# Performance work log

Hardware: AMD Instinct MI355X
Metric: run time of the kernel (lower is better)

The kernel has to match this reference:

```python
import jax, jax.numpy as jnp
import numpy as np

B, S, D, E = 16, 2048, 1024, 524288

def setup_inputs() -> dict:
    key = jax.random.key(0)
    k0, k1, k2, k3 = jax.random.split(key, 4)
    x = jax.random.normal(k0, (B, S, D), dtype=jnp.float32)
    mask = jnp.ones((B, S), dtype=bool)
    edges = jax.random.randint(k1, (2, E), 0, B * S, dtype=jnp.int32)
    scale = 1.0 / np.sqrt(D).astype(np.float32)
    W1 = jax.random.normal(k2, (D, D), dtype=jnp.float32) * scale  # GCNConv lin weight
    b1 = jnp.zeros((D,), dtype=jnp.float32)                        # GCNConv bias
    W2 = jax.random.normal(k3, (D, D), dtype=jnp.float32) * scale  # output Linear
    b2 = jnp.zeros((D,), dtype=jnp.float32)
    return {"x": x, "mask": mask, "edges": edges, "W1": W1, "b1": b1, "W2": W2, "b2": b2}

def reference(x, mask, edges, W1, b1, W2, b2):
    # x: [B,S,D]; mask all-True -> gather == reshape to [N,D]
    N = B * S
    nodes = x.reshape(N, D)
    src, dst = edges[0], edges[1]
    # GCN normalization (gcn_norm, add_self_loops=False): deg over dst, norm = d^-1/2[src]*d^-1/2[dst]
    deg = jax.ops.segment_sum(jnp.ones((E,), dtype=nodes.dtype), dst, num_segments=N)
    dinv = jnp.where(deg > 0, jax.lax.rsqrt(jnp.maximum(deg, 1e-12)), 0.0)
    norm = dinv[src] * dinv[dst]  # [E]
    h = nodes @ W1.T                                   # [N,D] transform
    msg = h[src] * norm[:, None]                       # [E,D] gather + scale
    agg = jax.ops.segment_sum(msg, dst, num_segments=N) + b1  # scatter-aggregate + bias
    g = jax.nn.gelu(agg, approximate=False)            # nn.GELU (exact erf)
    out = g @ W2.T + b2                                # Linear(graph_hid_dim -> input_dim)
    # residual scatter-add back into x (mask all True)
    return x + (out.reshape(B, S, D) * mask[:, :, None].astype(x.dtype))
```

## Files before the change

### kernel.cpp

```cpp
#include <hip/hip_runtime.h>
#include <hip/hip_fp8.h>
#include <stdint.h>

typedef unsigned short u16;
typedef __attribute__((ext_vector_type(8))) short s16x8;
typedef __attribute__((ext_vector_type(4))) float f32x4;
typedef __attribute__((ext_vector_type(2))) float f32x2;

#define D_DIM 1024
#define GK 1024
#define NT 16

__device__ __forceinline__ u16 f2bf(float f) {
  union { float f; uint32_t u; } v; v.f = f;
  uint32_t u = v.u;
  return (u16)((u + 0x7FFFu + ((u >> 16) & 1u)) >> 16);
}

__device__ __forceinline__ uint8_t f2fp8(float f) {
#if __has_builtin(__builtin_amdgcn_cvt_pk_fp8_f32)
  int p = __builtin_amdgcn_cvt_pk_fp8_f32(f, f, 0, false);
  return (uint8_t)(p & 0xff);
#else
  return __hip_fp8_e4m3(f).__x;
#endif
}


__device__ __forceinline__ int lds_half_off(int arr, int buf, int half) {
  return ((((arr << 1) | buf) << 1) | half) << 14;
}

__device__ __forceinline__ void stage_half(const u16* __restrict__ g, int rowBase, int kt,
                                           u16* lds, int arr, int buf, int half, int t) {
  const int hoff = lds_half_off(arr, buf, half);
#pragma unroll
  for (int j = 0; j < 2; ++j) {
    const int c = j * 512 + t;
    const int row = c >> 3;
    const int cb = (((c & 7) ^ (row & 7)) << 4);
    const u16* src = g + (size_t)(rowBase + half * 128 + row) * GK + kt * 64 + (cb >> 1);
    __builtin_amdgcn_global_load_lds((const __attribute__((address_space(1))) void*)src,
        (__attribute__((address_space(3))) void*)((char*)lds + hoff + c * 16), 16, 0, 0);
  }
}

template<int QM>
__device__ __forceinline__ void read_sub_a(const u16* lds, int buf, int half, int lane, s16x8* a) {
  const int base = lds_half_off(0, buf, half);
  const int rsel = lane & 15, cb0 = (lane >> 4) << 4;
#pragma unroll
  for (int im = 0; im < 4; ++im) {
    const int row = QM * 64 + im * 16 + rsel;
    const int swz = (row & 7) << 4;
#pragma unroll
    for (int ks = 0; ks < 2; ++ks)
      a[im * 2 + ks] = *(const s16x8*)((const char*)lds + base + row * 128 + ((ks * 64 + cb0) ^ swz));
  }
}

template<int QN>
__device__ __forceinline__ void read_sub_b(const u16* lds, int buf, int half, int rowBase, int lane, s16x8* b) {
  const int base = lds_half_off(1, buf, half);
  const int rsel = lane & 15, cb0 = (lane >> 4) << 4;
#pragma unroll
  for (int in_ = 0; in_ < 2; ++in_) {
    const int row = rowBase + (QN * 2 + in_) * 16 + rsel;
    const int swz = (row & 7) << 4;
#pragma unroll
    for (int ks = 0; ks < 2; ++ks)
      b[in_ * 2 + ks] = *(const s16x8*)((const char*)lds + base + row * 128 + ((ks * 64 + cb0) ^ swz));
  }
}

template<int QM, int QN>
__device__ __forceinline__ void do_quad(f32x4 acc[8][4], const s16x8* aS, const s16x8* bS) {
  __builtin_amdgcn_s_setprio(1);
#pragma unroll
  for (int im = 0; im < 4; ++im)
#pragma unroll
    for (int in_ = 0; in_ < 2; ++in_)
#pragma unroll
      for (int ks = 0; ks < 2; ++ks)
        acc[QM * 4 + im][QN * 2 + in_] = __builtin_amdgcn_mfma_f32_16x16x32_bf16(
            aS[im * 2 + ks], bS[in_ * 2 + ks], acc[QM * 4 + im][QN * 2 + in_], 0, 0, 0);
  __builtin_amdgcn_s_setprio(0);
}

#define BARRIER __builtin_amdgcn_s_barrier()
#define WAIT_LGKM asm volatile("s_waitcnt lgkmcnt(0)" ::: "memory")
#define WAIT_VM(n) asm volatile("s_waitcnt vmcnt(" #n ")" ::: "memory")

template<int EPI>
__global__ __launch_bounds__(512, 2) void gemm256(
    const u16* __restrict__ A, const u16* __restrict__ B, uint8_t* __restrict__ C8,
    const float* __restrict__ bias, const float* __restrict__ xres, float* __restrict__ Cf)
{
  __shared__ u16 lds[65536];
  const int t = threadIdx.x;
  const int lane = t & 63;
  const int w = t >> 6;
  const int wave_m = w >> 2;
  const int wave_n = w & 3;
  const int halfB = wave_n >> 1;
  const int rowBaseB = (wave_n & 1) * 64;

  const int lb = blockIdx.x;
  const int wid = ((lb & 7) << 6) | (lb >> 3);
  const int bm = wid >> 2;
  const int bn = wid & 3;
  const int rowA = bm * 256;
  const int rowB = bn * 256;

  f32x4 acc[8][4] = {};
  s16x8 aS[8], b0S[4], b1S[4];

  stage_half(A, rowA, 0, lds, 0, 0, 0, t);
  stage_half(A, rowA, 0, lds, 0, 0, 1, t);
  stage_half(B, rowB, 0, lds, 1, 0, 0, t);
  stage_half(B, rowB, 0, lds, 1, 0, 1, t);
  stage_half(B, rowB, 1, lds, 1, 1, 0, t);
  stage_half(B, rowB, 1, lds, 1, 1, 1, t);
  WAIT_VM(4);
  BARRIER;

  for (int i = 0; i < NT / 2 - 1; ++i) {
    const int t1 = 2 * i + 1;
    read_sub_a<0>(lds, 0, wave_m, lane, aS);
    read_sub_b<0>(lds, 0, halfB, rowBaseB, lane, b0S);
    stage_half(A, rowA, t1, lds, 0, 1, 0, t);
    BARRIER; WAIT_LGKM;
    do_quad<0, 0>(acc, aS, b0S);
    BARRIER;
    read_sub_b<1>(lds, 0, halfB, rowBaseB, lane, b1S);
    stage_half(A, rowA, t1, lds, 0, 1, 1, t);
    BARRIER; WAIT_LGKM;
    do_quad<0, 1>(acc, aS, b1S);
    BARRIER;
    read_sub_a<1>(lds, 0, wave_m, lane, aS);
    stage_half(B, rowB, 2 * i + 2, lds, 1, 0, 0, t);
    BARRIER; WAIT_LGKM;
    do_quad<1, 1>(acc, aS, b1S);
    BARRIER;
    stage_half(B, rowB, 2 * i + 2, lds, 1, 0, 1, t);
    WAIT_VM(4);
    BARRIER;
    do_quad<1, 0>(acc, aS, b0S);
    BARRIER;
    read_sub_a<0>(lds, 1, wave_m, lane, aS);
    read_sub_b<0>(lds, 1, halfB, rowBaseB, lane, b0S);
    stage_half(A, rowA, 2 * i + 2, lds, 0, 0, 0, t);
    BARRIER; WAIT_LGKM;
    do_quad<0, 0>(acc, aS, b0S);
    BARRIER;
    read_sub_b<1>(lds, 1, halfB, rowBaseB, lane, b1S);
    stage_half(A, rowA, 2 * i + 2, lds, 0, 0, 1, t);
    BARRIER; WAIT_LGKM;
    do_quad<0, 1>(acc, aS, b1S);
    BARRIER;
    read_sub_a<1>(lds, 1, wave_m, lane, aS);
    stage_half(B, rowB, 2 * i + 3, lds, 1, 1, 0, t);
    BARRIER; WAIT_LGKM;
    do_quad<1, 1>(acc, aS, b1S);
    BARRIER;
    stage_half(B, rowB, 2 * i + 3, lds, 1, 1, 1, t);
    WAIT_VM(4);
    BARRIER;
    do_quad<1, 0>(acc, aS, b0S);
    BARRIER;
  }

  {
    read_sub_a<0>(lds, 0, wave_m, lane, aS);
    read_sub_b<0>(lds, 0, halfB, rowBaseB, lane, b0S);
    stage_half(A, rowA, NT - 1, lds, 0, 1, 0, t);
    BARRIER; WAIT_LGKM;
    do_quad<0, 0>(acc, aS, b0S);
    BARRIER;
    read_sub_b<1>(lds, 0, halfB, rowBaseB, lane, b1S);
    stage_half(A, rowA, NT - 1, lds, 0, 1, 1, t);
    BARRIER; WAIT_LGKM;
    do_quad<0, 1>(acc, aS, b1S);
    BARRIER;
    read_sub_a<1>(lds, 0, wave_m, lane, aS);
    BARRIER; WAIT_LGKM;
    do_quad<1, 1>(acc, aS, b1S);
    BARRIER;
    WAIT_VM(0);
    BARRIER;
    do_quad<1, 0>(acc, aS, b0S);
    read_sub_a<0>(lds, 1, wave_m, lane, aS);
    read_sub_b<0>(lds, 1, halfB, rowBaseB, lane, b0S);
    WAIT_LGKM;
    do_quad<0, 0>(acc, aS, b0S);
    read_sub_b<1>(lds, 1, halfB, rowBaseB, lane, b1S);
    WAIT_LGKM;
    do_quad<0, 1>(acc, aS, b1S);
    read_sub_a<1>(lds, 1, wave_m, lane, aS);
    WAIT_LGKM;
    do_quad<1, 1>(acc, aS, b1S);
    do_quad<1, 0>(acc, aS, b0S);
  }

  const int row0 = rowA + wave_m * 128 + ((lane >> 4) << 2);
  const int col0 = rowB + wave_n * 64 + (lane & 15);
  if (EPI == 0) {
#pragma unroll
    for (int mf = 0; mf < 8; ++mf)
#pragma unroll
      for (int nf = 0; nf < 4; ++nf) {
        const int c = col0 + nf * 16;
#pragma unroll
        for (int r = 0; r < 4; ++r)
          C8[(size_t)(row0 + mf * 16 + r) * D_DIM + c] = f2fp8(acc[mf][nf][r]);
      }
  } else {
#pragma unroll
    for (int mf = 0; mf < 8; ++mf)
#pragma unroll
      for (int nf = 0; nf < 4; ++nf) {
        const int c = col0 + nf * 16;
        const float bv = bias[c];
#pragma unroll
        for (int r = 0; r < 4; ++r) {
          const size_t idx = (size_t)(row0 + mf * 16 + r) * D_DIM + c;
          Cf[idx] = acc[mf][nf][r] + bv + xres[idx];
        }
      }
  }
}

__global__ void cast_f32_bf16(const float* __restrict__ in, u16* __restrict__ out, long n) {
  long i = ((long)blockIdx.x * blockDim.x + threadIdx.x) * 4;
  if (i >= n) return;
  const float4 v = *(const float4*)(in + i);
  ushort4 o;
  o.x = f2bf(v.x); o.y = f2bf(v.y); o.z = f2bf(v.z); o.w = f2bf(v.w);
  *(ushort4*)(out + i) = o;
}

__global__ void deg_count_int(const int* __restrict__ dst, int* __restrict__ cnt, int E) {
  int i = blockIdx.x * blockDim.x + threadIdx.x;
  if (i < E) atomicAdd(&cnt[dst[i]], 1);
}

__global__ __launch_bounds__(1024) void scan_offsets(const int* __restrict__ cnt,
                                                     int* __restrict__ off,
                                                     int* __restrict__ cursor,
                                                     float* __restrict__ dinv, int N) {
  __shared__ int part[1024];
  const int t = threadIdx.x;
  const int nper = (N + 1023) / 1024;
  const int base = t * nper;
  int s = 0;
  for (int i = 0; i < nper; ++i) {
    int idx = base + i;
    if (idx < N) s += cnt[idx];
  }
  part[t] = s;
  __syncthreads();
  for (int d = 1; d < 1024; d <<= 1) {
    int v = (t >= d) ? part[t - d] : 0;
    __syncthreads();
    part[t] += v;
    __syncthreads();
  }
  int run = (t > 0) ? part[t - 1] : 0;
  for (int i = 0; i < nper; ++i) {
    int idx = base + i;
    if (idx < N) {
      const int c = cnt[idx];
      off[idx] = run;
      cursor[idx] = run;
      dinv[idx] = c > 0 ? rsqrtf((float)c) : 0.f;
      run += c;
    }
  }
  if (t == 1023) off[N] = run;
}

__global__ void fill_csr(const int* __restrict__ src, const int* __restrict__ dst,
                         const float* __restrict__ dinv, int* __restrict__ cursor,
                         uint2* __restrict__ ebuf, int E) {
  int e = blockIdx.x * blockDim.x + threadIdx.x;
  if (e >= E) return;
  const int d = dst[e], s = src[e];
  const int pos = atomicAdd(&cursor[d], 1);
  const float nrm = dinv[s] * dinv[d];
  uint2 en; en.x = (unsigned)s; en.y = __float_as_uint(nrm);
  ebuf[pos] = en;
}

__device__ __forceinline__ void acc8_fp8(float* a, uint2 hv, float nrm) {
#if __has_builtin(__builtin_amdgcn_cvt_pk_f32_fp8)
  const f32x2 p0 = __builtin_amdgcn_cvt_pk_f32_fp8(hv.x, false);
  const f32x2 p1 = __builtin_amdgcn_cvt_pk_f32_fp8(hv.x, true);
  const f32x2 p2 = __builtin_amdgcn_cvt_pk_f32_fp8(hv.y, false);
  const f32x2 p3 = __builtin_amdgcn_cvt_pk_f32_fp8(hv.y, true);
  a[0] += p0.x * nrm; a[1] += p0.y * nrm;
  a[2] += p1.x * nrm; a[3] += p1.y * nrm;
  a[4] += p2.x * nrm; a[5] += p2.y * nrm;
  a[6] += p3.x * nrm; a[7] += p3.y * nrm;
#else
  const float s = nrm * 0x1p+120f;
#pragma unroll
  for (int k = 0; k < 8; ++k) {
    const uint32_t word = (k < 4) ? hv.x : hv.y;
    const uint32_t b = (word >> ((k & 3) * 8)) & 0xffu;
    a[k] += __uint_as_float(((b & 0x80u) << 24) | ((b & 0x7fu) << 20)) * s;
  }
#endif
}

__device__ __forceinline__ float gelu_exact(float t) {
  return 0.5f * t * (1.0f + erff(t * 0.70710678118f));
}

__global__ __launch_bounds__(256) void aggregate_gelu_fp8(
    const uint8_t* __restrict__ h8, const uint2* __restrict__ ebuf,
    const int* __restrict__ off, const float* __restrict__ b1,
    u16* __restrict__ g)
{
  const int node = __builtin_amdgcn_readfirstlane(blockIdx.x * 2 + (threadIdx.x >> 7));
  const int lt = threadIdx.x & 127;
  const int fb = lt * 8;
  const int beg = off[node], end = off[node + 1];
  float a[8] = {0.f, 0.f, 0.f, 0.f, 0.f, 0.f, 0.f, 0.f};

  int i = beg;
  for (; i + 2 <= end; i += 2) {
    const uint2 ea = ebuf[i];
    const uint2 eb = ebuf[i + 1];
    const uint2 ha = *(const uint2*)(h8 + (size_t)ea.x * D_DIM + fb);
    const uint2 hb = *(const uint2*)(h8 + (size_t)eb.x * D_DIM + fb);
    acc8_fp8(a, ha, __uint_as_float(ea.y));
    acc8_fp8(a, hb, __uint_as_float(eb.y));
  }
  if (i < end) {
    const uint2 ea = ebuf[i];
    const uint2 ha = *(const uint2*)(h8 + (size_t)ea.x * D_DIM + fb);
    acc8_fp8(a, ha, __uint_as_float(ea.y));
  }

  const float4 bA = *(const float4*)(b1 + fb);
  const float4 bB = *(const float4*)(b1 + fb + 4);
  const float v0 = gelu_exact(a[0] + bA.x), v1 = gelu_exact(a[1] + bA.y);
  const float v2 = gelu_exact(a[2] + bA.z), v3 = gelu_exact(a[3] + bA.w);
  const float v4 = gelu_exact(a[4] + bB.x), v5 = gelu_exact(a[5] + bB.y);
  const float v6 = gelu_exact(a[6] + bB.z), v7 = gelu_exact(a[7] + bB.w);
  uint4 o;
  o.x = (uint32_t)f2bf(v0) | ((uint32_t)f2bf(v1) << 16);
  o.y = (uint32_t)f2bf(v2) | ((uint32_t)f2bf(v3) << 16);
  o.z = (uint32_t)f2bf(v4) | ((uint32_t)f2bf(v5) << 16);
  o.w = (uint32_t)f2bf(v6) | ((uint32_t)f2bf(v7) << 16);
  *(uint4*)(g + (size_t)node * D_DIM + fb) = o;
}

extern "C" void kernel_launch(void* const* d_in, const int* in_sizes, int n_in,
                              void* d_out, int out_size, void* d_ws, size_t ws_size,
                              hipStream_t stream) {
  const float* x  = (const float*)d_in[0];
  const int* edges = (const int*)d_in[2];
  const float* W1 = (const float*)d_in[3];
  const float* b1 = (const float*)d_in[4];
  const float* W2 = (const float*)d_in[5];
  const float* b2 = (const float*)d_in[6];
  float* out = (float*)d_out;

  const int D = D_DIM;
  const long ND = (long)in_sizes[0];
  const int N = (int)(ND / D);
  const int E = in_sizes[2] / 2;
  const int* src = edges;
  const int* dst = edges + E;

  u16* xbf    = (u16*)d_ws;
  uint8_t* h8 = (uint8_t*)(xbf + ND);
  u16* w1b    = (u16*)(h8 + ND);
  u16* w2b    = w1b + (size_t)D * D;
  int* cnt    = (int*)(w2b + (size_t)D * D);
  int* off    = cnt + N;
  int* cursor = off + N + 1;
  float* dnv  = (float*)(cursor + N);
  uint2* ebuf = (uint2*)(dnv + N + 1);

  hipMemsetAsync(cnt, 0, (size_t)N * sizeof(int), stream);

  cast_f32_bf16<<<(int)(ND / 4 / 256), 256, 0, stream>>>(x, xbf, ND);
  cast_f32_bf16<<<(int)((long)D * D / 4 / 256), 256, 0, stream>>>(W1, w1b, (long)D * D);
  cast_f32_bf16<<<(int)((long)D * D / 4 / 256), 256, 0, stream>>>(W2, w2b, (long)D * D);

  deg_count_int<<<(E + 255) / 256, 256, 0, stream>>>(dst, cnt, E);
  scan_offsets<<<1, 1024, 0, stream>>>(cnt, off, cursor, dnv, N);
  fill_csr<<<(E + 255) / 256, 256, 0, stream>>>(src, dst, dnv, cursor, ebuf, E);

  gemm256<0><<<(N / 256) * (D / 256), 512, 0, stream>>>(xbf, w1b, h8, nullptr, nullptr, nullptr);

  aggregate_gelu_fp8<<<N / 2, 256, 0, stream>>>(h8, ebuf, off, b1, xbf);

  gemm256<1><<<(N / 256) * (D / 256), 512, 0, stream>>>(xbf, w2b, nullptr, b2, x, out);
}
```

Baseline: 443.5 us.

## Make GEMM blocks persistent over two M-tiles with a continuous K pipeline

```diff
diff --git a/kernel.cpp b/kernel.cpp
--- a/kernel.cpp
+++ b/kernel.cpp
@@ -9,7 +9,7 @@
 
 #define D_DIM 1024
 #define GK 1024
-#define NT 16
+#define NT2 32
 
 __device__ __forceinline__ u16 f2bf(float f) {
   union { float f; uint32_t u; } v; v.f = f;
@@ -31,7 +31,7 @@
   return ((((arr << 1) | buf) << 1) | half) << 14;
 }
 
-__device__ __forceinline__ void stage_half(const u16* __restrict__ g, int rowBase, int kt,
+__device__ __forceinline__ void stage_half(const u16* __restrict__ g, int rowBase, int ktl,
                                            u16* lds, int arr, int buf, int half, int t) {
   const int hoff = lds_half_off(arr, buf, half);
 #pragma unroll
@@ -39,7 +39,7 @@
     const int c = j * 512 + t;
     const int row = c >> 3;
     const int cb = (((c & 7) ^ (row & 7)) << 4);
-    const u16* src = g + (size_t)(rowBase + half * 128 + row) * GK + kt * 64 + (cb >> 1);
+    const u16* src = g + (size_t)(rowBase + half * 128 + row) * GK + ktl * 64 + (cb >> 1);
     __builtin_amdgcn_global_load_lds((const __attribute__((address_space(1))) void*)src,
         (__attribute__((address_space(3))) void*)((char*)lds + hoff + c * 16), 16, 0, 0);
   }
@@ -90,6 +90,39 @@
 #define BARRIER __builtin_amdgcn_s_barrier()
 #define WAIT_LGKM asm volatile("s_waitcnt lgkmcnt(0)" ::: "memory")
 #define WAIT_VM(n) asm volatile("s_waitcnt vmcnt(" #n ")" ::: "memory")
+
+template<int EPI>
+__device__ __forceinline__ void write_tile(const f32x4 (&acc)[8][4], int rowBase, int colBase,
+    uint8_t* __restrict__ C8, const float* __restrict__ bias, const float* __restrict__ xres,
+    float* __restrict__ Cf, int lane, int wave_m, int wave_n)
+{
+  const int row0 = rowBase + wave_m * 128 + ((lane >> 4) << 2);
+  const int col0 = colBase + wave_n * 64 + (lane & 15);
+  if (EPI == 0) {
+#pragma unroll
+    for (int mf = 0; mf < 8; ++mf)
+#pragma unroll
+      for (int nf = 0; nf < 4; ++nf) {
+        const int c = col0 + nf * 16;
+#pragma unroll
+        for (int r = 0; r < 4; ++r)
+          C8[(size_t)(row0 + mf * 16 + r) * D_DIM + c] = f2fp8(acc[mf][nf][r]);
+      }
+  } else {
+#pragma unroll
+    for (int mf = 0; mf < 8; ++mf)
+#pragma unroll
+      for (int nf = 0; nf < 4; ++nf) {
+        const int c = col0 + nf * 16;
+        const float bv = bias[c];
+#pragma unroll
+        for (int r = 0; r < 4; ++r) {
+          const size_t idx = (size_t)(row0 + mf * 16 + r) * D_DIM + c;
+          Cf[idx] = acc[mf][nf][r] + bv + xres[idx];
+        }
+      }
+  }
+}
 
 template<int EPI>
 __global__ __launch_bounds__(512, 2) void gemm256(
@@ -105,80 +138,92 @@
   const int halfB = wave_n >> 1;
   const int rowBaseB = (wave_n & 1) * 64;
 
-  const int lb = blockIdx.x;
-  const int wid = ((lb & 7) << 6) | (lb >> 3);
-  const int bm = wid >> 2;
-  const int bn = wid & 3;
-  const int rowA = bm * 256;
-  const int rowB = bn * 256;
+  const int b = blockIdx.x;
+  const int bn = b & 3;
+  const int q  = b >> 2;
+  const int rowA0 = (2 * q) * 256;
+  const int rowA1 = (2 * q + 1) * 256;
+  const int rowB  = bn * 256;
 
   f32x4 acc[8][4] = {};
   s16x8 aS[8], b0S[4], b1S[4];
 
-  stage_half(A, rowA, 0, lds, 0, 0, 0, t);
-  stage_half(A, rowA, 0, lds, 0, 0, 1, t);
-  stage_half(B, rowB, 0, lds, 1, 0, 0, t);
-  stage_half(B, rowB, 0, lds, 1, 0, 1, t);
-  stage_half(B, rowB, 1, lds, 1, 1, 0, t);
-  stage_half(B, rowB, 1, lds, 1, 1, 1, t);
+#define STAGE_A(kt, buf, half) stage_half(A, ((kt) & 16) ? rowA1 : rowA0, (kt) & 15, lds, 0, buf, half, t)
+#define STAGE_B(kt, buf, half) stage_half(B, rowB, (kt) & 15, lds, 1, buf, half, t)
+
+  STAGE_A(0, 0, 0);
+  STAGE_A(0, 0, 1);
+  STAGE_B(0, 0, 0);
+  STAGE_B(0, 0, 1);
+  STAGE_B(1, 1, 0);
+  STAGE_B(1, 1, 1);
   WAIT_VM(4);
   BARRIER;
 
-  for (int i = 0; i < NT / 2 - 1; ++i) {
-    const int t1 = 2 * i + 1;
+  for (int i = 0; i < NT2 / 2 - 1; ++i) {
+    const int t1 = 2 * i + 1, u0 = 2 * i + 2, u1 = 2 * i + 3;
     read_sub_a<0>(lds, 0, wave_m, lane, aS);
     read_sub_b<0>(lds, 0, halfB, rowBaseB, lane, b0S);
-    stage_half(A, rowA, t1, lds, 0, 1, 0, t);
+    STAGE_A(t1, 1, 0);
     BARRIER; WAIT_LGKM;
     do_quad<0, 0>(acc, aS, b0S);
     BARRIER;
     read_sub_b<1>(lds, 0, halfB, rowBaseB, lane, b1S);
-    stage_half(A, rowA, t1, lds, 0, 1, 1, t);
+    STAGE_A(t1, 1, 1);
     BARRIER; WAIT_LGKM;
     do_quad<0, 1>(acc, aS, b1S);
     BARRIER;
     read_sub_a<1>(lds, 0, wave_m, lane, aS);
-    stage_half(B, rowB, 2 * i + 2, lds, 1, 0, 0, t);
+    STAGE_B(u0, 0, 0);
     BARRIER; WAIT_LGKM;
     do_quad<1, 1>(acc, aS, b1S);
     BARRIER;
-    stage_half(B, rowB, 2 * i + 2, lds, 1, 0, 1, t);
+    STAGE_B(u0, 0, 1);
+    BARRIER;
+    do_quad<1, 0>(acc, aS, b0S);
     WAIT_VM(4);
-    BARRIER;
-    do_quad<1, 0>(acc, aS, b0S);
     BARRIER;
     read_sub_a<0>(lds, 1, wave_m, lane, aS);
     read_sub_b<0>(lds, 1, halfB, rowBaseB, lane, b0S);
-    stage_half(A, rowA, 2 * i + 2, lds, 0, 0, 0, t);
+    STAGE_A(u0, 0, 0);
     BARRIER; WAIT_LGKM;
     do_quad<0, 0>(acc, aS, b0S);
     BARRIER;
     read_sub_b<1>(lds, 1, halfB, rowBaseB, lane, b1S);
-    stage_half(A, rowA, 2 * i + 2, lds, 0, 0, 1, t);
+    STAGE_A(u0, 0, 1);
     BARRIER; WAIT_LGKM;
     do_quad<0, 1>(acc, aS, b1S);
     BARRIER;
     read_sub_a<1>(lds, 1, wave_m, lane, aS);
-    stage_half(B, rowB, 2 * i + 3, lds, 1, 1, 0, t);
+    STAGE_B(u1, 1, 0);
     BARRIER; WAIT_LGKM;
     do_quad<1, 1>(acc, aS, b1S);
     BARRIER;
-    stage_half(B, rowB, 2 * i + 3, lds, 1, 1, 1, t);
+    STAGE_B(u1, 1, 1);
+    BARRIER;
+    do_quad<1, 0>(acc, aS, b0S);
     WAIT_VM(4);
     BARRIER;
-    do_quad<1, 0>(acc, aS, b0S);
-    BARRIER;
+
+    if (i == 7) {
+      write_tile<EPI>(acc, rowA0, rowB, C8, bias, xres, Cf, lane, wave_m, wave_n);
+#pragma unroll
+      for (int mf = 0; mf < 8; ++mf)
+#pragma unroll
+        for (int nf = 0; nf < 4; ++nf)
+          acc[mf][nf] = (f32x4){0.f, 0.f, 0.f, 0.f};
+    }
   }
 
   {
     read_sub_a<0>(lds, 0, wave_m, lane, aS);
     read_sub_b<0>(lds, 0, halfB, rowBaseB, lane, b0S);
-    stage_half(A, rowA, NT - 1, lds, 0, 1, 0, t);
+    STAGE_A(NT2 - 1, 1, 0);
     BARRIER; WAIT_LGKM;
     do_quad<0, 0>(acc, aS, b0S);
     BARRIER;
     read_sub_b<1>(lds, 0, halfB, rowBaseB, lane, b1S);
-    stage_half(A, rowA, NT - 1, lds, 0, 1, 1, t);
+    STAGE_A(NT2 - 1, 1, 1);
     BARRIER; WAIT_LGKM;
     do_quad<0, 1>(acc, aS, b1S);
     BARRIER;
@@ -202,32 +247,9 @@
     do_quad<1, 0>(acc, aS, b0S);
   }
 
-  const int row0 = rowA + wave_m * 128 + ((lane >> 4) << 2);
-  const int col0 = rowB + wave_n * 64 + (lane & 15);
-  if (EPI == 0) {
-#pragma unroll
-    for (int mf = 0; mf < 8; ++mf)
-#pragma unroll
-      for (int nf = 0; nf < 4; ++nf) {
-        const int c = col0 + nf * 16;
-#pragma unroll
-        for (int r = 0; r < 4; ++r)
-          C8[(size_t)(row0 + mf * 16 + r) * D_DIM + c] = f2fp8(acc[mf][nf][r]);
-      }
-  } else {
-#pragma unroll
-    for (int mf = 0; mf < 8; ++mf)
-#pragma unroll
-      for (int nf = 0; nf < 4; ++nf) {
-        const int c = col0 + nf * 16;
-        const float bv = bias[c];
-#pragma unroll
-        for (int r = 0; r < 4; ++r) {
-          const size_t idx = (size_t)(row0 + mf * 16 + r) * D_DIM + c;
-          Cf[idx] = acc[mf][nf][r] + bv + xres[idx];
-        }
-      }
-  }
+  write_tile<EPI>(acc, rowA1, rowB, C8, bias, xres, Cf, lane, wave_m, wave_n);
+#undef STAGE_A
+#undef STAGE_B
 }
 
 __global__ void cast_f32_bf16(const float* __restrict__ in, u16* __restrict__ out, long n) {
@@ -394,9 +416,9 @@
   scan_offsets<<<1, 1024, 0, stream>>>(cnt, off, cursor, dnv, N);
   fill_csr<<<(E + 255) / 256, 256, 0, stream>>>(src, dst, dnv, cursor, ebuf, E);
 
-  gemm256<0><<<(N / 256) * (D / 256), 512, 0, stream>>>(xbf, w1b, h8, nullptr, nullptr, nullptr);
+  gemm256<0><<<256, 512, 0, stream>>>(xbf, w1b, h8, nullptr, nullptr, nullptr);
 
   aggregate_gelu_fp8<<<N / 2, 256, 0, stream>>>(h8, ebuf, off, b1, xbf);
 
-  gemm256<1><<<(N / 256) * (D / 256), 512, 0, stream>>>(xbf, w2b, nullptr, b2, x, out);
-}
+  gemm256<1><<<256, 512, 0, stream>>>(xbf, w2b, nullptr, b2, x, out);
+}
```

After: 577.2 us. 30.1% more time.
